# Kernel tuning notes

Measured on AMD Instinct MI355X. Metric: run time of the kernel, lower is better.

## Reference

```python
import jax, jax.numpy as jnp
import numpy as np

_EPS = 1e-5

def _ln(x, scale, shift):
    # Faithful to the module's custom layer norm: variance term is the SUM of
    # squared deviations over the feature dim (not the mean), and the affine is
    # scale * normed + shift with scale=b*, shift=s* (argument order as in source).
    m = jnp.mean(x, axis=-1, keepdims=True)
    d = x - m
    ssq = jnp.sum(d * d, axis=-1, keepdims=True)
    return scale * (d / jnp.sqrt(ssq + _EPS)) + shift


def setup_inputs() -> dict:
    key = jax.random.key(0)
    ks = jax.random.split(key, 12)
    B, T, I, H = 64, 512, 512, 512
    f32 = jnp.float32
    return {
        "x": jax.random.normal(ks[0], (B, T, I), f32),
        "hx": jax.random.normal(ks[1], (B, H), f32),
        "cx": jax.random.normal(ks[2], (B, H), f32),
        "Wi": jax.random.normal(ks[3], (4 * H, I), f32) / np.float32(np.sqrt(I)),
        "Wh": jax.random.normal(ks[4], (4 * H, H), f32) / np.float32(np.sqrt(H)),
        "bias": jax.random.normal(ks[5], (4 * H,), f32) * 0.1,
        "b1": jax.random.normal(ks[6], (4 * H,), f32) * 0.1,
        "b2": jax.random.normal(ks[7], (4 * H,), f32) * 0.1,
        "b3": jax.random.normal(ks[8], (H,), f32) * 0.1,
        "s1": 1.0 + jax.random.normal(ks[9], (4 * H,), f32) * 0.1,
        "s2": 1.0 + jax.random.normal(ks[10], (4 * H,), f32) * 0.1,
        "s3": 1.0 + jax.random.normal(ks[11], (H,), f32) * 0.1,
    }


def reference(x, hx, cx, Wi, Wh, bias, b1, b2, b3, s1, s2, s3):
    # x: [B, T, I] (batch_first). Work in time-major for the scan.
    xT = jnp.swapaxes(x, 0, 1)  # [T, B, I]
    # The input-projection layer norm has no cross-time dependency -> precompute.
    gi = _ln(jnp.einsum('tbi,gi->tbg', xT, Wi), b1, s1)  # [T, B, 4H]

    def step(carry, gi_t):
        h, c = carry
        gates = gi_t + _ln(h @ Wh.T, b2, s2) + bias  # [B, 4H]
        i, f, g, o = jnp.split(gates, 4, axis=-1)
        i = jax.nn.sigmoid(i)
        f = jax.nn.sigmoid(f)
        g = jnp.tanh(g)
        o = jax.nn.sigmoid(o)
        c_new = _ln(f * c + i * g, b3, s3)
        h_new = o * jnp.tanh(c_new)
        return (h_new, c_new), h_new

    (hy, cy), ys = jax.lax.scan(step, (hx, cx), gi)
    output = jnp.swapaxes(ys, 0, 1)  # back to [B, T, H]
    return output, hy, cy
```

## Files before the change

kernel.cpp:

```cpp
#include <hip/hip_runtime.h>
#include <cstdint>
#include <cstddef>


typedef float  f32x4 __attribute__((ext_vector_type(4)));
typedef __bf16 bf16x8 __attribute__((ext_vector_type(8)));
typedef unsigned int u32x4 __attribute__((ext_vector_type(4)));
typedef unsigned short u16x4 __attribute__((ext_vector_type(4)));

#define DEV __device__ __forceinline__

DEV unsigned short f2b(float f){
  unsigned int u = __builtin_bit_cast(unsigned int, f);
  unsigned int r = (u + 0x7FFFu + ((u >> 16) & 1u)) >> 16;
  return (unsigned short)r;
}
DEV float b2f(unsigned short s){
  unsigned int u = ((unsigned int)s) << 16;
  return __builtin_bit_cast(float, u);
}
DEV float tanh_fast(float x){
  const float e = __expf(2.f * x);
  return 1.f - 2.f * __builtin_amdgcn_rcpf(e + 1.f);
}
DEV float sigmoid_fast(float x){
  return __builtin_amdgcn_rcpf(1.f + __expf(-x));
}

__global__ __launch_bounds__(256) void conv_bf16(const float* __restrict__ src,
                                                 unsigned short* __restrict__ dst,
                                                 int n4){
  int i = blockIdx.x * 256 + threadIdx.x;
  if (i >= n4) return;
  f32x4 v = ((const f32x4*)src)[i];
  u16x4 o;
  #pragma unroll
  for (int j = 0; j < 4; ++j) o[j] = f2b(v[j]);
  ((u16x4*)dst)[i] = o;
}

__global__ __launch_bounds__(256) void init_h(const float* __restrict__ hx,
                                              unsigned long long* __restrict__ hbuf){
  int s = blockIdx.x;
  int p = threadIdx.x;
  float h0 = hx[s * 512 + 2 * p];
  float h1 = hx[s * 512 + 2 * p + 1];
  unsigned long long v = (unsigned long long)f2b(h0) |
                         ((unsigned long long)f2b(h1) << 16);
  hbuf[(size_t)s * 512 + p] = v;
}

__global__ __launch_bounds__(256, 2) void gemm_gi(const unsigned short* __restrict__ Xb,
                                                  const unsigned short* __restrict__ Wib,
                                                  unsigned short* __restrict__ Gp){
  __shared__ unsigned short As[128 * 48];
  __shared__ unsigned short Bs[128 * 48];
  const int tid = threadIdx.x;
  const int m0 = blockIdx.x * 128;
  const int n0 = blockIdx.y * 128;
  const int w = tid >> 6, lane = tid & 63;
  const int lr = lane & 15, lq = lane >> 4;
  const int wm = (w & 1) * 64, wn = (w >> 1) * 64;
  const int sr = tid >> 2;
  const int sc = (tid & 3) * 8;
  const unsigned short* gx = Xb + (size_t)(m0 + sr) * 512 + sc;
  const unsigned short* gw = Wib + (size_t)(n0 + sr) * 512 + sc;
  f32x4 acc[4][4] = {};
  for (int kb = 0; kb < 16; ++kb){
    u32x4 a0 = *(const u32x4*)(gx + kb * 32);
    u32x4 a1 = *(const u32x4*)(gx + 64 * 512 + kb * 32);
    u32x4 b0 = *(const u32x4*)(gw + kb * 32);
    u32x4 b1 = *(const u32x4*)(gw + 64 * 512 + kb * 32);
    __syncthreads();
    *(u32x4*)&As[sr * 48 + sc] = a0;
    *(u32x4*)&As[(sr + 64) * 48 + sc] = a1;
    *(u32x4*)&Bs[sr * 48 + sc] = b0;
    *(u32x4*)&Bs[(sr + 64) * 48 + sc] = b1;
    __syncthreads();
    bf16x8 af[4], bfv[4];
    #pragma unroll
    for (int mi = 0; mi < 4; ++mi) af[mi] = *(const bf16x8*)&As[(wm + mi * 16 + lr) * 48 + lq * 8];
    #pragma unroll
    for (int ni = 0; ni < 4; ++ni) bfv[ni] = *(const bf16x8*)&Bs[(wn + ni * 16 + lr) * 48 + lq * 8];
    #pragma unroll
    for (int mi = 0; mi < 4; ++mi)
      #pragma unroll
      for (int ni = 0; ni < 4; ++ni)
        acc[mi][ni] = __builtin_amdgcn_mfma_f32_16x16x32_bf16(af[mi], bfv[ni], acc[mi][ni], 0, 0, 0);
  }
  #pragma unroll
  for (int mi = 0; mi < 4; ++mi){
    const int rowb = m0 + wm + mi * 16 + lq * 4;
    #pragma unroll
    for (int ni = 0; ni < 4; ++ni){
      const int col = n0 + wn + ni * 16 + lr;
      #pragma unroll
      for (int r = 0; r < 4; ++r)
        Gp[(size_t)(rowb + r) * 2048 + col] = f2b(acc[mi][ni][r]);
    }
  }
}

__global__ __launch_bounds__(256) void ln_rows(unsigned short* __restrict__ G,
                                               const float* __restrict__ b1,
                                               const float* __restrict__ s1){
  const int row = blockIdx.x;
  const int tid = threadIdx.x;
  unsigned short* rp = G + (size_t)row * 2048 + tid * 8;
  u32x4 raw = *(const u32x4*)rp;
  float x[8];
  #pragma unroll
  for (int j = 0; j < 8; ++j){
    unsigned int word = raw[j >> 1];
    unsigned short us = (j & 1) ? (unsigned short)(word >> 16) : (unsigned short)(word & 0xFFFF);
    x[j] = b2f(us);
  }
  float s = 0.f, q = 0.f;
  #pragma unroll
  for (int j = 0; j < 8; ++j){ s += x[j]; q += x[j] * x[j]; }
  #pragma unroll
  for (int o = 1; o < 64; o <<= 1){ s += __shfl_xor(s, o); q += __shfl_xor(q, o); }
  __shared__ float ps[4][2];
  const int wv = tid >> 6;
  if ((tid & 63) == 0){ ps[wv][0] = s; ps[wv][1] = q; }
  __syncthreads();
  s = ps[0][0] + ps[1][0] + ps[2][0] + ps[3][0];
  q = ps[0][1] + ps[1][1] + ps[2][1] + ps[3][1];
  const float mu = s * (1.f / 2048.f);
  const float inv = rsqrtf((q - s * mu) + 1e-5f);
  const float* b1p = b1 + tid * 8;
  const float* s1p = s1 + tid * 8;
  u32x4 outw;
  #pragma unroll
  for (int j = 0; j < 4; ++j){
    float y0 = b1p[2 * j]     * ((x[2 * j]     - mu) * inv) + s1p[2 * j];
    float y1 = b1p[2 * j + 1] * ((x[2 * j + 1] - mu) * inv) + s1p[2 * j + 1];
    outw[j] = (unsigned int)f2b(y0) | ((unsigned int)f2b(y1) << 16);
  }
  *(u32x4*)rp = outw;
}

__global__ __launch_bounds__(512, 2) void lstm_rec(
    const unsigned short* __restrict__ Gi,
    const unsigned short* __restrict__ Whb,
    const float* __restrict__ bias,
    const float* __restrict__ b2, const float* __restrict__ s2,
    const float* __restrict__ b3, const float* __restrict__ s3,
    const float* __restrict__ cx,
    unsigned long long* __restrict__ hbuf,
    unsigned long long* __restrict__ pA,
    unsigned long long* __restrict__ pCs,
    float* __restrict__ out){
  const int tid = threadIdx.x;
  const int tm = (blockIdx.x >> 1) & 3;
  const int ks = ((blockIdx.x >> 3) << 1) | (blockIdx.x & 1);
  const int w = tid >> 6;
  const int lane = tid & 63;
  const int lr = lane & 15, lq = lane >> 4;

  const int type = w >> 1;
  const int jloc = (w & 1) * 16 + lr;
  const int row_g = type * 512 + ks * 32 + jloc;
  const float b2r = b2[row_g];
  const float sbr = s2[row_g] + bias[row_g];

  bf16x8 bfr[16];
  {
    const unsigned short* wr = Whb + (size_t)row_g * 512 + lq * 8;
    #pragma unroll
    for (int kk = 0; kk < 16; ++kk) bfr[kk] = *(const bf16x8*)(wr + kk * 32);
  }

  const int cs = tid >> 5;
  const int cj = tid & 31;
  const int hcol = ks * 32 + cj;
  const int bidx = tm * 16 + cs;
  float c_val = cx[(size_t)bidx * 512 + hcol];
  const float b3j = b3[hcol], s3j = s3[hcol];

  const int psmp = 2 * w + (lane >> 5);
  const int pidx = lane & 31;
  const int pl_slice = (lane >> 1) & 15;
  const int pl_kind  = lane & 1;

  float b3c[16], s3c[16];
  #pragma unroll
  for (int jj = 0; jj < 8; ++jj){
    const int c0 = 2 * pidx + 64 * jj;
    b3c[2 * jj]     = b3[c0];     b3c[2 * jj + 1] = b3[c0 + 1];
    s3c[2 * jj]     = s3[c0];     s3c[2 * jj + 1] = s3[c0 + 1];
  }

  __shared__ unsigned short hlds[16 * 520];
  __shared__ float act[4][32][17];
  __shared__ float redA[8][16][2];
  __shared__ float stAl[16][2];

  float cc_own = 0.f, o_own = 0.f;

  for (int t = 0; t < 512; ++t){
    float giv[4];
    #pragma unroll
    for (int r = 0; r < 4; ++r){
      const int b = tm * 16 + lq * 4 + r;
      giv[r] = b2f(Gi[((size_t)b * 512 + t) * 2048 + row_g]);
    }

    if (t == 0){
      const unsigned long long* hsrc = hbuf + (size_t)(tm * 16 + psmp) * 512;
      unsigned long long hv[8];
      for (;;){
        bool ok = true;
        #pragma unroll
        for (int j = 0; j < 8; ++j)
          hv[j] = __hip_atomic_load(hsrc + pidx + 32 * j, __ATOMIC_RELAXED, __HIP_MEMORY_SCOPE_AGENT);
        #pragma unroll
        for (int j = 0; j < 8; ++j) ok &= ((unsigned)(hv[j] >> 32) == 0u);
        if (__all((int)ok)) break;
      }
      #pragma unroll
      for (int j = 0; j < 8; ++j)
        *(unsigned int*)&hlds[psmp * 520 + 2 * (pidx + 32 * j)] = (unsigned)hv[j];
    } else {
      const unsigned int tg = (unsigned)t;
      const unsigned long long* hsrc =
          hbuf + (size_t)(t & 1) * 32768 + (size_t)(tm * 16 + psmp) * 512;
      const unsigned long long* sp =
          pCs + ((size_t)(t & 1) * 4 + tm) * 512 + pl_slice * 32 + psmp * 2 + pl_kind;
      unsigned long long hv[16];
      unsigned long long sv;
      for (;;){
        bool ok = true;
        #pragma unroll
        for (int j = 0; j < 16; ++j)
          hv[j] = __hip_atomic_load(hsrc + 2 * pidx + 64 * (j >> 1) + (j & 1),
                                    __ATOMIC_RELAXED, __HIP_MEMORY_SCOPE_AGENT);
        sv = __hip_atomic_load(sp, __ATOMIC_RELAXED, __HIP_MEMORY_SCOPE_AGENT);
        #pragma unroll
        for (int j = 0; j < 16; ++j) ok &= ((unsigned)(hv[j] >> 32) == tg);
        ok &= ((unsigned)(sv >> 32) == tg);
        if (__all((int)ok)) break;
      }
      float pv = __builtin_bit_cast(float, (unsigned)sv);
      #pragma unroll
      for (int o = 2; o < 32; o <<= 1) pv += __shfl_xor(pv, o);
      const float ov = __shfl_xor(pv, 1);
      const float S = pl_kind ? ov : pv;
      const float Q = pl_kind ? pv : ov;
      const float mu = S * (1.f / 512.f);
      const float inv = rsqrtf((Q - S * mu) + 1e-5f);
      c_val = b3j * ((cc_own - mu) * inv) + s3j;
      const float h_self = o_own * tanh_fast(c_val);
      out[((size_t)bidx * 512 + (t - 1)) * 512 + hcol] = h_self;
      #pragma unroll
      for (int jj = 0; jj < 8; ++jj){
        const unsigned long long v0 = hv[2 * jj], v1 = hv[2 * jj + 1];
        const float cc0 = b2f((unsigned short)(v0 & 0xFFFF));
        const float oo0 = b2f((unsigned short)((v0 >> 16) & 0xFFFF));
        const float cc1 = b2f((unsigned short)(v1 & 0xFFFF));
        const float oo1 = b2f((unsigned short)((v1 >> 16) & 0xFFFF));
        const float h0 = oo0 * tanh_fast(b3c[2 * jj]     * ((cc0 - mu) * inv) + s3c[2 * jj]);
        const float h1 = oo1 * tanh_fast(b3c[2 * jj + 1] * ((cc1 - mu) * inv) + s3c[2 * jj + 1]);
        *(unsigned int*)&hlds[psmp * 520 + 2 * pidx + 64 * jj] =
            (unsigned)f2b(h0) | ((unsigned)f2b(h1) << 16);
      }
    }
    __syncthreads();

    f32x4 acc = {0.f, 0.f, 0.f, 0.f};
    #pragma unroll
    for (int kk = 0; kk < 16; ++kk){
      bf16x8 af = *(const bf16x8*)&hlds[lr * 520 + lq * 8 + kk * 32];
      acc = __builtin_amdgcn_mfma_f32_16x16x32_bf16(af, bfr[kk], acc, 0, 0, 0);
    }
    #pragma unroll
    for (int r = 0; r < 4; ++r){
      float s = acc[r], q = acc[r] * acc[r];
      #pragma unroll
      for (int o = 1; o < 16; o <<= 1){ s += __shfl_xor(s, o); q += __shfl_xor(q, o); }
      if (lr == 0){ redA[w][lq * 4 + r][0] = s; redA[w][lq * 4 + r][1] = q; }
    }
    __syncthreads();

    unsigned long long* slotA = pA + ((size_t)(t & 1) * 4 + tm) * 512;
    const unsigned int atag = (unsigned)(t + 1);
    if (w == 0 && lane < 32){
      const int smp = lane >> 1, kd = lane & 1;
      float Sp = 0.f;
      #pragma unroll
      for (int w2 = 0; w2 < 8; ++w2) Sp += redA[w2][smp][kd];
      const unsigned long long pvs = ((unsigned long long)atag << 32) |
          (unsigned long long)__builtin_bit_cast(unsigned int, Sp);
      __hip_atomic_store(slotA + (size_t)ks * 32 + lane, pvs,
                         __ATOMIC_RELAXED, __HIP_MEMORY_SCOPE_AGENT);
    }
    {
      const unsigned long long* ap = slotA + pl_slice * 32 + psmp * 2 + pl_kind;
      unsigned long long av;
      for (;;){
        av = __hip_atomic_load(ap, __ATOMIC_RELAXED, __HIP_MEMORY_SCOPE_AGENT);
        if (__all((int)((unsigned)(av >> 32) == atag))) break;
      }
      float pv = __builtin_bit_cast(float, (unsigned)av);
      #pragma unroll
      for (int o = 2; o < 32; o <<= 1) pv += __shfl_xor(pv, o);
      const float ov = __shfl_xor(pv, 1);
      const float S = pl_kind ? ov : pv;
      const float Q = pl_kind ? pv : ov;
      if ((lane & 31) == 0){
        const float mu = S * (1.f / 2048.f);
        stAl[psmp][0] = mu;
        stAl[psmp][1] = rsqrtf((Q - S * mu) + 1e-5f);
      }
    }
    __syncthreads();

    #pragma unroll
    for (int r = 0; r < 4; ++r){
      const int s0 = lq * 4 + r;
      const float nv = (acc[r] - stAl[s0][0]) * stAl[s0][1];
      const float gv = giv[r] + b2r * nv + sbr;
      float a;
      if (type == 2) a = tanh_fast(gv);
      else           a = sigmoid_fast(gv);
      act[type][jloc][s0] = a;
    }
    __syncthreads();

    const float i_g = act[0][cj][cs];
    const float f_g = act[1][cj][cs];
    const float g_g = act[2][cj][cs];
    const float o_g = act[3][cj][cs];
    const float cc = f_g * c_val + i_g * g_g;
    float sC = cc, qC = cc * cc;
    #pragma unroll
    for (int o = 1; o < 32; o <<= 1){ sC += __shfl_xor(sC, o); qC += __shfl_xor(qC, o); }

    const unsigned int ntag = (unsigned)(t + 1);
    const size_t np = (size_t)((t + 1) & 1);
    unsigned long long* slotC = pCs + (np * 4 + tm) * 512;
    if ((lane & 31) < 2){
      const float v = (lane & 1) ? qC : sC;
      const unsigned long long pvs = ((unsigned long long)ntag << 32) |
          (unsigned long long)__builtin_bit_cast(unsigned int, v);
      __hip_atomic_store(slotC + (size_t)ks * 32 + cs * 2 + (lane & 1), pvs,
                         __ATOMIC_RELAXED, __HIP_MEMORY_SCOPE_AGENT);
    }
    {
      const unsigned long long pvh = ((unsigned long long)ntag << 32) |
          (unsigned long long)f2b(cc) | ((unsigned long long)f2b(o_g) << 16);
      __hip_atomic_store(hbuf + np * 32768 + (size_t)bidx * 512 + hcol, pvh,
                         __ATOMIC_RELAXED, __HIP_MEMORY_SCOPE_AGENT);
    }
    cc_own = cc; o_own = o_g;
  }

  {
    const unsigned long long* sp =
        pCs + ((size_t)0 * 4 + tm) * 512 + pl_slice * 32 + psmp * 2 + pl_kind;
    unsigned long long sv;
    for (;;){
      sv = __hip_atomic_load(sp, __ATOMIC_RELAXED, __HIP_MEMORY_SCOPE_AGENT);
      if (__all((int)((unsigned)(sv >> 32) == 512u))) break;
    }
    float pv = __builtin_bit_cast(float, (unsigned)sv);
    #pragma unroll
    for (int o = 2; o < 32; o <<= 1) pv += __shfl_xor(pv, o);
    const float ov = __shfl_xor(pv, 1);
    const float S = pl_kind ? ov : pv;
    const float Q = pl_kind ? pv : ov;
    const float mu = S * (1.f / 512.f);
    const float inv = rsqrtf((Q - S * mu) + 1e-5f);
    const float cn = b3j * ((cc_own - mu) * inv) + s3j;
    const float h = o_own * tanh_fast(cn);
    out[((size_t)bidx * 512 + 511) * 512 + hcol] = h;
    out[16777216u + (size_t)bidx * 512 + hcol] = h;
    out[16777216u + 32768u + (size_t)bidx * 512 + hcol] = cn;
  }
}

extern "C" void kernel_launch(void* const* d_in, const int* in_sizes, int n_in,
                              void* d_out, int out_size, void* d_ws, size_t ws_size,
                              hipStream_t stream){
  (void)in_sizes; (void)n_in; (void)out_size; (void)ws_size;
  const float* x    = (const float*)d_in[0];
  const float* hx   = (const float*)d_in[1];
  const float* cx   = (const float*)d_in[2];
  const float* Wi   = (const float*)d_in[3];
  const float* Wh   = (const float*)d_in[4];
  const float* bias = (const float*)d_in[5];
  const float* b1   = (const float*)d_in[6];
  const float* b2   = (const float*)d_in[7];
  const float* b3   = (const float*)d_in[8];
  const float* s1   = (const float*)d_in[9];
  const float* s2   = (const float*)d_in[10];
  const float* s3   = (const float*)d_in[11];
  float* out = (float*)d_out;
  char* ws = (char*)d_ws;

  unsigned short*     xb   = (unsigned short*)(ws);
  unsigned short*     wib  = (unsigned short*)(ws + 33554432);
  unsigned short*     whb  = (unsigned short*)(ws + 35651584);
  unsigned short*     gp   = (unsigned short*)(ws + 37748736);
  unsigned long long* hbuf = (unsigned long long*)(ws + 171966464);
  unsigned long long* pA   = (unsigned long long*)(ws + 172490752);
  unsigned long long* pCs  = (unsigned long long*)(ws + 172523520);

  hipMemsetAsync(hbuf, 0, 589824, stream);
  conv_bf16<<<16384, 256, 0, stream>>>(x,  xb,  4194304);
  conv_bf16<<<1024,  256, 0, stream>>>(Wi, wib, 262144);
  conv_bf16<<<1024,  256, 0, stream>>>(Wh, whb, 262144);
  init_h<<<64, 256, 0, stream>>>(hx, hbuf);
  gemm_gi<<<dim3(256, 16, 1), 256, 0, stream>>>(xb, wib, gp);
  ln_rows<<<32768, 256, 0, stream>>>(gp, b1, s1);
  lstm_rec<<<64, 512, 0, stream>>>(gp, whb, bias, b2, s2, b3, s3, cx,
                                   hbuf, pA, pCs, out);
}
```

Baseline: 3.590 ms.

## Group recurrent blocks per XCD and poll peers via sc0 loads

```diff
diff --git a/kernel.cpp b/kernel.cpp
--- a/kernel.cpp
+++ b/kernel.cpp
@@ -10,6 +10,14 @@
 
 #define DEV __device__ __forceinline__
 
+#define LD2_SC0(dst, p) asm volatile("global_load_dwordx2 %0, %1, off sc0" : "=v"(dst) : "v"(p))
+#define ST2_SC0(p, v)   asm volatile("global_store_dwordx2 %0, %1, off sc0" :: "v"(p), "v"(v) : "memory")
+#define LD2_MALL(dst, p) (dst) = __hip_atomic_load((p), __ATOMIC_RELAXED, __HIP_MEMORY_SCOPE_AGENT)
+#define VM0_FENCE() do{ asm volatile("s_waitcnt vmcnt(0)" ::: "memory"); \
+                        __builtin_amdgcn_sched_barrier(0); }while(0)
+
+#define NBLK 320
+
 DEV unsigned short f2b(float f){
   unsigned int u = __builtin_bit_cast(unsigned int, f);
   unsigned int r = (u + 0x7FFFu + ((u >> 16) & 1u)) >> 16;
@@ -25,6 +33,10 @@
 }
 DEV float sigmoid_fast(float x){
   return __builtin_amdgcn_rcpf(1.f + __expf(-x));
+}
+DEV void post_u64(unsigned long long* p, unsigned long long v){
+  ST2_SC0(p, v);
+  __hip_atomic_store(p, v, __ATOMIC_RELAXED, __HIP_MEMORY_SCOPE_AGENT);
 }
 
 __global__ __launch_bounds__(256) void conv_bf16(const float* __restrict__ src,
@@ -150,10 +162,47 @@
     unsigned long long* __restrict__ hbuf,
     unsigned long long* __restrict__ pA,
     unsigned long long* __restrict__ pCs,
+    unsigned int* __restrict__ form,
     float* __restrict__ out){
   const int tid = threadIdx.x;
-  const int tm = (blockIdx.x >> 1) & 3;
-  const int ks = ((blockIdx.x >> 3) << 1) | (blockIdx.x & 1);
+
+  __shared__ int s_tm, s_ks;
+  if (tid == 0){
+    const unsigned xcd = __builtin_amdgcn_s_getreg((31 << 11) | 20) & 15u;
+    const unsigned k = __hip_atomic_fetch_add(&form[xcd], 1u,
+                          __ATOMIC_RELAXED, __HIP_MEMORY_SCOPE_AGENT);
+    const unsigned c = k >> 4, m = k & 15u;
+    unsigned int* gcnt = &form[16 + xcd * 20 + c];
+    unsigned int* tqp  = &form[336 + xcd * 20 + c];
+    __hip_atomic_fetch_add(gcnt, 1u, __ATOMIC_RELAXED, __HIP_MEMORY_SCOPE_AGENT);
+    __hip_atomic_fetch_add(&form[656], 1u, __ATOMIC_RELEASE, __HIP_MEMORY_SCOPE_AGENT);
+    if (m == 0){
+      unsigned g;
+      for (;;){
+        g = __hip_atomic_load(gcnt, __ATOMIC_RELAXED, __HIP_MEMORY_SCOPE_AGENT);
+        if (g >= 16u) break;
+        unsigned a = __hip_atomic_load(&form[656], __ATOMIC_ACQUIRE, __HIP_MEMORY_SCOPE_AGENT);
+        if (a >= (unsigned)NBLK){
+          g = __hip_atomic_load(gcnt, __ATOMIC_RELAXED, __HIP_MEMORY_SCOPE_AGENT);
+          break;
+        }
+      }
+      unsigned tq = 255u;
+      if (g >= 16u)
+        tq = __hip_atomic_fetch_add(&form[657], 1u, __ATOMIC_RELAXED, __HIP_MEMORY_SCOPE_AGENT);
+      __hip_atomic_store(tqp, tq | 0x100u, __ATOMIC_RELAXED, __HIP_MEMORY_SCOPE_AGENT);
+    }
+    unsigned v;
+    do { v = __hip_atomic_load(tqp, __ATOMIC_RELAXED, __HIP_MEMORY_SCOPE_AGENT); }
+    while (!(v & 0x100u));
+    s_tm = (int)(v & 0xFFu);
+    s_ks = (int)m;
+  }
+  __syncthreads();
+  const int tm = s_tm;
+  const int ks = s_ks;
+  if (tm >= 4) return;
+
   const int w = tid >> 6;
   const int lane = tid & 63;
   const int lr = lane & 15, lq = lane >> 4;
@@ -197,6 +246,7 @@
   __shared__ float stAl[16][2];
 
   float cc_own = 0.f, o_own = 0.f;
+  bool use_mall = false;
 
   for (int t = 0; t < 512; ++t){
     float giv[4];
@@ -208,19 +258,26 @@
 
     if (t == 0){
       const unsigned long long* hsrc = hbuf + (size_t)(tm * 16 + psmp) * 512;
-      unsigned long long hv[8];
+      unsigned long long hv0[8];
+      unsigned spin = 0;
       for (;;){
+        if (!use_mall){
+          #pragma unroll
+          for (int j = 0; j < 8; ++j) LD2_SC0(hv0[j], hsrc + pidx + 32 * j);
+          VM0_FENCE();
+        } else {
+          #pragma unroll
+          for (int j = 0; j < 8; ++j) LD2_MALL(hv0[j], hsrc + pidx + 32 * j);
+        }
         bool ok = true;
         #pragma unroll
-        for (int j = 0; j < 8; ++j)
-          hv[j] = __hip_atomic_load(hsrc + pidx + 32 * j, __ATOMIC_RELAXED, __HIP_MEMORY_SCOPE_AGENT);
-        #pragma unroll
-        for (int j = 0; j < 8; ++j) ok &= ((unsigned)(hv[j] >> 32) == 0u);
+        for (int j = 0; j < 8; ++j) ok &= ((unsigned)(hv0[j] >> 32) == 0u);
         if (__all((int)ok)) break;
+        if (++spin > 64u) use_mall = true;
       }
       #pragma unroll
       for (int j = 0; j < 8; ++j)
-        *(unsigned int*)&hlds[psmp * 520 + 2 * (pidx + 32 * j)] = (unsigned)hv[j];
+        *(unsigned int*)&hlds[psmp * 520 + 2 * (pidx + 32 * j)] = (unsigned)hv0[j];
     } else {
       const unsigned int tg = (unsigned)t;
       const unsigned long long* hsrc =
@@ -229,17 +286,26 @@
           pCs + ((size_t)(t & 1) * 4 + tm) * 512 + pl_slice * 32 + psmp * 2 + pl_kind;
       unsigned long long hv[16];
       unsigned long long sv;
+      unsigned spin = 0;
       for (;;){
+        if (!use_mall){
+          #pragma unroll
+          for (int j = 0; j < 16; ++j)
+            LD2_SC0(hv[j], hsrc + 2 * pidx + 64 * (j >> 1) + (j & 1));
+          LD2_SC0(sv, sp);
+          VM0_FENCE();
+        } else {
+          #pragma unroll
+          for (int j = 0; j < 16; ++j)
+            LD2_MALL(hv[j], hsrc + 2 * pidx + 64 * (j >> 1) + (j & 1));
+          LD2_MALL(sv, sp);
+        }
         bool ok = true;
-        #pragma unroll
-        for (int j = 0; j < 16; ++j)
-          hv[j] = __hip_atomic_load(hsrc + 2 * pidx + 64 * (j >> 1) + (j & 1),
-                                    __ATOMIC_RELAXED, __HIP_MEMORY_SCOPE_AGENT);
-        sv = __hip_atomic_load(sp, __ATOMIC_RELAXED, __HIP_MEMORY_SCOPE_AGENT);
         #pragma unroll
         for (int j = 0; j < 16; ++j) ok &= ((unsigned)(hv[j] >> 32) == tg);
         ok &= ((unsigned)(sv >> 32) == tg);
         if (__all((int)ok)) break;
+        if (++spin > 64u) use_mall = true;
       }
       float pv = __builtin_bit_cast(float, (unsigned)sv);
       #pragma unroll
@@ -291,15 +357,17 @@
       for (int w2 = 0; w2 < 8; ++w2) Sp += redA[w2][smp][kd];
       const unsigned long long pvs = ((unsigned long long)atag << 32) |
           (unsigned long long)__builtin_bit_cast(unsigned int, Sp);
-      __hip_atomic_store(slotA + (size_t)ks * 32 + lane, pvs,
-                         __ATOMIC_RELAXED, __HIP_MEMORY_SCOPE_AGENT);
+      post_u64(slotA + (size_t)ks * 32 + lane, pvs);
     }
     {
       const unsigned long long* ap = slotA + pl_slice * 32 + psmp * 2 + pl_kind;
       unsigned long long av;
+      unsigned spin = 0;
       for (;;){
-        av = __hip_atomic_load(ap, __ATOMIC_RELAXED, __HIP_MEMORY_SCOPE_AGENT);
+        if (!use_mall){ LD2_SC0(av, ap); VM0_FENCE(); }
+        else          { LD2_MALL(av, ap); }
         if (__all((int)((unsigned)(av >> 32) == atag))) break;
+        if (++spin > 64u) use_mall = true;
       }
       float pv = __builtin_bit_cast(float, (unsigned)av);
       #pragma unroll
@@ -343,14 +411,12 @@
       const float v = (lane & 1) ? qC : sC;
       const unsigned long long pvs = ((unsigned long long)ntag << 32) |
           (unsigned long long)__builtin_bit_cast(unsigned int, v);
-      __hip_atomic_store(slotC + (size_t)ks * 32 + cs * 2 + (lane & 1), pvs,
-                         __ATOMIC_RELAXED, __HIP_MEMORY_SCOPE_AGENT);
+      post_u64(slotC + (size_t)ks * 32 + cs * 2 + (lane & 1), pvs);
     }
     {
       const unsigned long long pvh = ((unsigned long long)ntag << 32) |
           (unsigned long long)f2b(cc) | ((unsigned long long)f2b(o_g) << 16);
-      __hip_atomic_store(hbuf + np * 32768 + (size_t)bidx * 512 + hcol, pvh,
-                         __ATOMIC_RELAXED, __HIP_MEMORY_SCOPE_AGENT);
+      post_u64(hbuf + np * 32768 + (size_t)bidx * 512 + hcol, pvh);
     }
     cc_own = cc; o_own = o_g;
   }
@@ -359,9 +425,12 @@
     const unsigned long long* sp =
         pCs + ((size_t)0 * 4 + tm) * 512 + pl_slice * 32 + psmp * 2 + pl_kind;
     unsigned long long sv;
+    unsigned spin = 0;
     for (;;){
-      sv = __hip_atomic_load(sp, __ATOMIC_RELAXED, __HIP_MEMORY_SCOPE_AGENT);
+      if (!use_mall){ LD2_SC0(sv, sp); VM0_FENCE(); }
+      else          { LD2_MALL(sv, sp); }
       if (__all((int)((unsigned)(sv >> 32) == 512u))) break;
+      if (++spin > 64u) use_mall = true;
     }
     float pv = __builtin_bit_cast(float, (unsigned)sv);
     #pragma unroll
@@ -405,14 +474,15 @@
   unsigned long long* hbuf = (unsigned long long*)(ws + 171966464);
   unsigned long long* pA   = (unsigned long long*)(ws + 172490752);
   unsigned long long* pCs  = (unsigned long long*)(ws + 172523520);
-
-  hipMemsetAsync(hbuf, 0, 589824, stream);
+  unsigned int*       form = (unsigned int*)(ws + 172556288);
+
+  hipMemsetAsync(hbuf, 0, 593920, stream);
   conv_bf16<<<16384, 256, 0, stream>>>(x,  xb,  4194304);
   conv_bf16<<<1024,  256, 0, stream>>>(Wi, wib, 262144);
   conv_bf16<<<1024,  256, 0, stream>>>(Wh, whb, 262144);
   init_h<<<64, 256, 0, stream>>>(hx, hbuf);
   gemm_gi<<<dim3(256, 16, 1), 256, 0, stream>>>(xb, wib, gp);
   ln_rows<<<32768, 256, 0, stream>>>(gp, b1, s1);
-  lstm_rec<<<64, 512, 0, stream>>>(gp, whb, bias, b2, s2, b3, s3, cx,
-                                   hbuf, pA, pCs, out);
-}
+  lstm_rec<<<NBLK, 512, 0, stream>>>(gp, whb, bias, b2, s2, b3, s3, cx,
+                                     hbuf, pA, pCs, form, out);
+}
```

New measurement: 4.130 ms. +15.0%, slower.

## Vectorize spin-wait polling, add sleep backoff, publish h earlier, pad LDS for occupancy

Applied to the files above, without the earlier changes.

```diff
diff --git a/kernel.cpp b/kernel.cpp
--- a/kernel.cpp
+++ b/kernel.cpp
@@ -7,8 +7,13 @@
 typedef __bf16 bf16x8 __attribute__((ext_vector_type(8)));
 typedef unsigned int u32x4 __attribute__((ext_vector_type(4)));
 typedef unsigned short u16x4 __attribute__((ext_vector_type(4)));
+typedef unsigned long long u64x2 __attribute__((ext_vector_type(2)));
 
 #define DEV __device__ __forceinline__
+
+#define LD4_AGENT(dst, p) asm volatile("global_load_dwordx4 %0, %1, off sc1" : "=v"(dst) : "v"(p))
+#define VM0_FENCE() do{ asm volatile("s_waitcnt vmcnt(0)" ::: "memory"); \
+                        __builtin_amdgcn_sched_barrier(0); }while(0)
 
 DEV unsigned short f2b(float f){
   unsigned int u = __builtin_bit_cast(unsigned int, f);
@@ -195,8 +200,11 @@
   __shared__ float act[4][32][17];
   __shared__ float redA[8][16][2];
   __shared__ float stAl[16][2];
+  __shared__ char occ_pad[60 * 1024];
+  if (blockIdx.x == 0xFFFFu) occ_pad[tid] = (char)tid;
 
   float cc_own = 0.f, o_own = 0.f;
+  bool use_mall = false;
 
   for (int t = 0; t < 512; ++t){
     float giv[4];
@@ -208,19 +216,20 @@
 
     if (t == 0){
       const unsigned long long* hsrc = hbuf + (size_t)(tm * 16 + psmp) * 512;
-      unsigned long long hv[8];
+      unsigned long long hv0[8];
       for (;;){
         bool ok = true;
         #pragma unroll
         for (int j = 0; j < 8; ++j)
-          hv[j] = __hip_atomic_load(hsrc + pidx + 32 * j, __ATOMIC_RELAXED, __HIP_MEMORY_SCOPE_AGENT);
+          hv0[j] = __hip_atomic_load(hsrc + pidx + 32 * j, __ATOMIC_RELAXED, __HIP_MEMORY_SCOPE_AGENT);
         #pragma unroll
-        for (int j = 0; j < 8; ++j) ok &= ((unsigned)(hv[j] >> 32) == 0u);
+        for (int j = 0; j < 8; ++j) ok &= ((unsigned)(hv0[j] >> 32) == 0u);
         if (__all((int)ok)) break;
+        __builtin_amdgcn_s_sleep(2);
       }
       #pragma unroll
       for (int j = 0; j < 8; ++j)
-        *(unsigned int*)&hlds[psmp * 520 + 2 * (pidx + 32 * j)] = (unsigned)hv[j];
+        *(unsigned int*)&hlds[psmp * 520 + 2 * (pidx + 32 * j)] = (unsigned)hv0[j];
     } else {
       const unsigned int tg = (unsigned)t;
       const unsigned long long* hsrc =
@@ -229,17 +238,30 @@
           pCs + ((size_t)(t & 1) * 4 + tm) * 512 + pl_slice * 32 + psmp * 2 + pl_kind;
       unsigned long long hv[16];
       unsigned long long sv;
+      unsigned spin = 0;
       for (;;){
         bool ok = true;
-        #pragma unroll
-        for (int j = 0; j < 16; ++j)
-          hv[j] = __hip_atomic_load(hsrc + 2 * pidx + 64 * (j >> 1) + (j & 1),
-                                    __ATOMIC_RELAXED, __HIP_MEMORY_SCOPE_AGENT);
-        sv = __hip_atomic_load(sp, __ATOMIC_RELAXED, __HIP_MEMORY_SCOPE_AGENT);
+        if (!use_mall){
+          u64x2 t4[8];
+          #pragma unroll
+          for (int q = 0; q < 8; ++q) LD4_AGENT(t4[q], hsrc + 2 * pidx + 64 * q);
+          sv = __hip_atomic_load(sp, __ATOMIC_RELAXED, __HIP_MEMORY_SCOPE_AGENT);
+          VM0_FENCE();
+          #pragma unroll
+          for (int q = 0; q < 8; ++q){ hv[2 * q] = t4[q].x; hv[2 * q + 1] = t4[q].y; }
+        } else {
+          #pragma unroll
+          for (int j = 0; j < 16; ++j)
+            hv[j] = __hip_atomic_load(hsrc + 2 * pidx + 64 * (j >> 1) + (j & 1),
+                                      __ATOMIC_RELAXED, __HIP_MEMORY_SCOPE_AGENT);
+          sv = __hip_atomic_load(sp, __ATOMIC_RELAXED, __HIP_MEMORY_SCOPE_AGENT);
+        }
         #pragma unroll
         for (int j = 0; j < 16; ++j) ok &= ((unsigned)(hv[j] >> 32) == tg);
         ok &= ((unsigned)(sv >> 32) == tg);
         if (__all((int)ok)) break;
+        if (++spin > 48u) use_mall = true;
+        __builtin_amdgcn_s_sleep(2);
       }
       float pv = __builtin_bit_cast(float, (unsigned)sv);
       #pragma unroll
@@ -300,6 +322,7 @@
       for (;;){
         av = __hip_atomic_load(ap, __ATOMIC_RELAXED, __HIP_MEMORY_SCOPE_AGENT);
         if (__all((int)((unsigned)(av >> 32) == atag))) break;
+        __builtin_amdgcn_s_sleep(2);
       }
       float pv = __builtin_bit_cast(float, (unsigned)av);
       #pragma unroll
@@ -332,12 +355,17 @@
     const float g_g = act[2][cj][cs];
     const float o_g = act[3][cj][cs];
     const float cc = f_g * c_val + i_g * g_g;
-    float sC = cc, qC = cc * cc;
-    #pragma unroll
-    for (int o = 1; o < 32; o <<= 1){ sC += __shfl_xor(sC, o); qC += __shfl_xor(qC, o); }
-
     const unsigned int ntag = (unsigned)(t + 1);
     const size_t np = (size_t)((t + 1) & 1);
+    {
+      const unsigned long long pvh = ((unsigned long long)ntag << 32) |
+          (unsigned long long)f2b(cc) | ((unsigned long long)f2b(o_g) << 16);
+      __hip_atomic_store(hbuf + np * 32768 + (size_t)bidx * 512 + hcol, pvh,
+                         __ATOMIC_RELAXED, __HIP_MEMORY_SCOPE_AGENT);
+    }
+    float sC = cc, qC = cc * cc;
+    #pragma unroll
+    for (int o = 1; o < 32; o <<= 1){ sC += __shfl_xor(sC, o); qC += __shfl_xor(qC, o); }
     unsigned long long* slotC = pCs + (np * 4 + tm) * 512;
     if ((lane & 31) < 2){
       const float v = (lane & 1) ? qC : sC;
@@ -346,12 +374,6 @@
       __hip_atomic_store(slotC + (size_t)ks * 32 + cs * 2 + (lane & 1), pvs,
                          __ATOMIC_RELAXED, __HIP_MEMORY_SCOPE_AGENT);
     }
-    {
-      const unsigned long long pvh = ((unsigned long long)ntag << 32) |
-          (unsigned long long)f2b(cc) | ((unsigned long long)f2b(o_g) << 16);
-      __hip_atomic_store(hbuf + np * 32768 + (size_t)bidx * 512 + hcol, pvh,
-                         __ATOMIC_RELAXED, __HIP_MEMORY_SCOPE_AGENT);
-    }
     cc_own = cc; o_own = o_g;
   }
 
@@ -362,6 +384,7 @@
     for (;;){
       sv = __hip_atomic_load(sp, __ATOMIC_RELAXED, __HIP_MEMORY_SCOPE_AGENT);
       if (__all((int)((unsigned)(sv >> 32) == 512u))) break;
+      __builtin_amdgcn_s_sleep(2);
     }
     float pv = __builtin_bit_cast(float, (unsigned)sv);
     #pragma unroll
```

Result: faster. 2.969 ms (-17.3%).

## Replace per-element tagged h exchange with per-block flags plus bulk payload loads

Applied to the files above, without the earlier changes.

```diff
diff --git a/kernel.cpp b/kernel.cpp
--- a/kernel.cpp
+++ b/kernel.cpp
@@ -9,6 +9,10 @@
 typedef unsigned short u16x4 __attribute__((ext_vector_type(4)));
 
 #define DEV __device__ __forceinline__
+
+#define LD4_AGENT(dst, p) asm volatile("global_load_dwordx4 %0, %1, off sc1" : "=v"(dst) : "v"(p))
+#define VM0_FENCE() do{ asm volatile("s_waitcnt vmcnt(0)" ::: "memory"); \
+                        __builtin_amdgcn_sched_barrier(0); }while(0)
 
 DEV unsigned short f2b(float f){
   unsigned int u = __builtin_bit_cast(unsigned int, f);
@@ -37,17 +41,6 @@
   #pragma unroll
   for (int j = 0; j < 4; ++j) o[j] = f2b(v[j]);
   ((u16x4*)dst)[i] = o;
-}
-
-__global__ __launch_bounds__(256) void init_h(const float* __restrict__ hx,
-                                              unsigned long long* __restrict__ hbuf){
-  int s = blockIdx.x;
-  int p = threadIdx.x;
-  float h0 = hx[s * 512 + 2 * p];
-  float h1 = hx[s * 512 + 2 * p + 1];
-  unsigned long long v = (unsigned long long)f2b(h0) |
-                         ((unsigned long long)f2b(h1) << 16);
-  hbuf[(size_t)s * 512 + p] = v;
 }
 
 __global__ __launch_bounds__(256, 2) void gemm_gi(const unsigned short* __restrict__ Xb,
@@ -146,8 +139,10 @@
     const float* __restrict__ bias,
     const float* __restrict__ b2, const float* __restrict__ s2,
     const float* __restrict__ b3, const float* __restrict__ s3,
+    const float* __restrict__ hx,
     const float* __restrict__ cx,
-    unsigned long long* __restrict__ hbuf,
+    unsigned int* __restrict__ hbuf,
+    unsigned long long* __restrict__ pF,
     unsigned long long* __restrict__ pA,
     unsigned long long* __restrict__ pCs,
     float* __restrict__ out){
@@ -185,11 +180,13 @@
 
   float b3c[16], s3c[16];
   #pragma unroll
-  for (int jj = 0; jj < 8; ++jj){
-    const int c0 = 2 * pidx + 64 * jj;
-    b3c[2 * jj]     = b3[c0];     b3c[2 * jj + 1] = b3[c0 + 1];
-    s3c[2 * jj]     = s3[c0];     s3c[2 * jj + 1] = s3[c0 + 1];
-  }
+  for (int q = 0; q < 4; ++q)
+    #pragma unroll
+    for (int j = 0; j < 4; ++j){
+      const int c = 4 * pidx + 128 * q + j;
+      b3c[4 * q + j] = b3[c];
+      s3c[4 * q + j] = s3[c];
+    }
 
   __shared__ unsigned short hlds[16 * 520];
   __shared__ float act[4][32][17];
@@ -207,40 +204,34 @@
     }
 
     if (t == 0){
-      const unsigned long long* hsrc = hbuf + (size_t)(tm * 16 + psmp) * 512;
-      unsigned long long hv[8];
-      for (;;){
-        bool ok = true;
+      const float* hr = hx + (size_t)(tm * 16 + psmp) * 512;
+      #pragma unroll
+      for (int q = 0; q < 4; ++q){
+        f32x4 hv4 = *(const f32x4*)(hr + 4 * pidx + 128 * q);
+        unsigned long long pk = 0;
         #pragma unroll
-        for (int j = 0; j < 8; ++j)
-          hv[j] = __hip_atomic_load(hsrc + pidx + 32 * j, __ATOMIC_RELAXED, __HIP_MEMORY_SCOPE_AGENT);
-        #pragma unroll
-        for (int j = 0; j < 8; ++j) ok &= ((unsigned)(hv[j] >> 32) == 0u);
-        if (__all((int)ok)) break;
+        for (int j = 0; j < 4; ++j)
+          pk |= (unsigned long long)f2b(hv4[j]) << (16 * j);
+        *(unsigned long long*)&hlds[psmp * 520 + 4 * pidx + 128 * q] = pk;
       }
-      #pragma unroll
-      for (int j = 0; j < 8; ++j)
-        *(unsigned int*)&hlds[psmp * 520 + 2 * (pidx + 32 * j)] = (unsigned)hv[j];
     } else {
       const unsigned int tg = (unsigned)t;
-      const unsigned long long* hsrc =
-          hbuf + (size_t)(t & 1) * 32768 + (size_t)(tm * 16 + psmp) * 512;
+      const unsigned long long* fp = pF + (size_t)(t & 1) * 64 + tm * 16 + (lane & 15);
       const unsigned long long* sp =
           pCs + ((size_t)(t & 1) * 4 + tm) * 512 + pl_slice * 32 + psmp * 2 + pl_kind;
-      unsigned long long hv[16];
       unsigned long long sv;
       for (;;){
-        bool ok = true;
-        #pragma unroll
-        for (int j = 0; j < 16; ++j)
-          hv[j] = __hip_atomic_load(hsrc + 2 * pidx + 64 * (j >> 1) + (j & 1),
-                                    __ATOMIC_RELAXED, __HIP_MEMORY_SCOPE_AGENT);
+        unsigned long long fv = __hip_atomic_load(fp, __ATOMIC_RELAXED, __HIP_MEMORY_SCOPE_AGENT);
         sv = __hip_atomic_load(sp, __ATOMIC_RELAXED, __HIP_MEMORY_SCOPE_AGENT);
-        #pragma unroll
-        for (int j = 0; j < 16; ++j) ok &= ((unsigned)(hv[j] >> 32) == tg);
-        ok &= ((unsigned)(sv >> 32) == tg);
+        bool ok = ((unsigned)fv == tg) & ((unsigned)(sv >> 32) == tg);
         if (__all((int)ok)) break;
+        __builtin_amdgcn_s_sleep(1);
       }
+      const unsigned int* hsrc =
+          hbuf + (size_t)(t & 1) * 32768 + (size_t)(tm * 16 + psmp) * 512;
+      u32x4 pay[4];
+      #pragma unroll
+      for (int q = 0; q < 4; ++q) LD4_AGENT(pay[q], hsrc + 4 * pidx + 128 * q);
       float pv = __builtin_bit_cast(float, (unsigned)sv);
       #pragma unroll
       for (int o = 2; o < 32; o <<= 1) pv += __shfl_xor(pv, o);
@@ -252,17 +243,19 @@
       c_val = b3j * ((cc_own - mu) * inv) + s3j;
       const float h_self = o_own * tanh_fast(c_val);
       out[((size_t)bidx * 512 + (t - 1)) * 512 + hcol] = h_self;
-      #pragma unroll
-      for (int jj = 0; jj < 8; ++jj){
-        const unsigned long long v0 = hv[2 * jj], v1 = hv[2 * jj + 1];
-        const float cc0 = b2f((unsigned short)(v0 & 0xFFFF));
-        const float oo0 = b2f((unsigned short)((v0 >> 16) & 0xFFFF));
-        const float cc1 = b2f((unsigned short)(v1 & 0xFFFF));
-        const float oo1 = b2f((unsigned short)((v1 >> 16) & 0xFFFF));
-        const float h0 = oo0 * tanh_fast(b3c[2 * jj]     * ((cc0 - mu) * inv) + s3c[2 * jj]);
-        const float h1 = oo1 * tanh_fast(b3c[2 * jj + 1] * ((cc1 - mu) * inv) + s3c[2 * jj + 1]);
-        *(unsigned int*)&hlds[psmp * 520 + 2 * pidx + 64 * jj] =
-            (unsigned)f2b(h0) | ((unsigned)f2b(h1) << 16);
+      VM0_FENCE();
+      #pragma unroll
+      for (int q = 0; q < 4; ++q){
+        unsigned long long pk = 0;
+        #pragma unroll
+        for (int j = 0; j < 4; ++j){
+          const unsigned int v = pay[q][j];
+          const float ccv = b2f((unsigned short)(v & 0xFFFF));
+          const float oov = b2f((unsigned short)(v >> 16));
+          const float h = oov * tanh_fast(b3c[4 * q + j] * ((ccv - mu) * inv) + s3c[4 * q + j]);
+          pk |= (unsigned long long)f2b(h) << (16 * j);
+        }
+        *(unsigned long long*)&hlds[psmp * 520 + 4 * pidx + 128 * q] = pk;
       }
     }
     __syncthreads();
@@ -300,6 +293,7 @@
       for (;;){
         av = __hip_atomic_load(ap, __ATOMIC_RELAXED, __HIP_MEMORY_SCOPE_AGENT);
         if (__all((int)((unsigned)(av >> 32) == atag))) break;
+        __builtin_amdgcn_s_sleep(2);
       }
       float pv = __builtin_bit_cast(float, (unsigned)av);
       #pragma unroll
@@ -332,12 +326,16 @@
     const float g_g = act[2][cj][cs];
     const float o_g = act[3][cj][cs];
     const float cc = f_g * c_val + i_g * g_g;
-    float sC = cc, qC = cc * cc;
-    #pragma unroll
-    for (int o = 1; o < 32; o <<= 1){ sC += __shfl_xor(sC, o); qC += __shfl_xor(qC, o); }
-
     const unsigned int ntag = (unsigned)(t + 1);
     const size_t np = (size_t)((t + 1) & 1);
+    {
+      const unsigned int pv32 = (unsigned int)f2b(cc) | ((unsigned int)f2b(o_g) << 16);
+      __hip_atomic_store(hbuf + np * 32768 + (size_t)bidx * 512 + hcol, pv32,
+                         __ATOMIC_RELAXED, __HIP_MEMORY_SCOPE_AGENT);
+    }
+    float sC = cc, qC = cc * cc;
+    #pragma unroll
+    for (int o = 1; o < 32; o <<= 1){ sC += __shfl_xor(sC, o); qC += __shfl_xor(qC, o); }
     unsigned long long* slotC = pCs + (np * 4 + tm) * 512;
     if ((lane & 31) < 2){
       const float v = (lane & 1) ? qC : sC;
@@ -346,12 +344,11 @@
       __hip_atomic_store(slotC + (size_t)ks * 32 + cs * 2 + (lane & 1), pvs,
                          __ATOMIC_RELAXED, __HIP_MEMORY_SCOPE_AGENT);
     }
-    {
-      const unsigned long long pvh = ((unsigned long long)ntag << 32) |
-          (unsigned long long)f2b(cc) | ((unsigned long long)f2b(o_g) << 16);
-      __hip_atomic_store(hbuf + np * 32768 + (size_t)bidx * 512 + hcol, pvh,
+    VM0_FENCE();
+    __syncthreads();
+    if (tid == 0)
+      __hip_atomic_store(pF + np * 64 + tm * 16 + ks, (unsigned long long)ntag,
                          __ATOMIC_RELAXED, __HIP_MEMORY_SCOPE_AGENT);
-    }
     cc_own = cc; o_own = o_g;
   }
 
@@ -362,6 +359,7 @@
     for (;;){
       sv = __hip_atomic_load(sp, __ATOMIC_RELAXED, __HIP_MEMORY_SCOPE_AGENT);
       if (__all((int)((unsigned)(sv >> 32) == 512u))) break;
+      __builtin_amdgcn_s_sleep(2);
     }
     float pv = __builtin_bit_cast(float, (unsigned)sv);
     #pragma unroll
@@ -402,17 +400,17 @@
   unsigned short*     wib  = (unsigned short*)(ws + 33554432);
   unsigned short*     whb  = (unsigned short*)(ws + 35651584);
   unsigned short*     gp   = (unsigned short*)(ws + 37748736);
-  unsigned long long* hbuf = (unsigned long long*)(ws + 171966464);
+  unsigned int*       hbuf = (unsigned int*)(ws + 171966464);
+  unsigned long long* pF   = (unsigned long long*)(ws + 172228608);
   unsigned long long* pA   = (unsigned long long*)(ws + 172490752);
   unsigned long long* pCs  = (unsigned long long*)(ws + 172523520);
 
-  hipMemsetAsync(hbuf, 0, 589824, stream);
+  hipMemsetAsync(pF, 0, 327680, stream);
   conv_bf16<<<16384, 256, 0, stream>>>(x,  xb,  4194304);
   conv_bf16<<<1024,  256, 0, stream>>>(Wi, wib, 262144);
   conv_bf16<<<1024,  256, 0, stream>>>(Wh, whb, 262144);
-  init_h<<<64, 256, 0, stream>>>(hx, hbuf);
   gemm_gi<<<dim3(256, 16, 1), 256, 0, stream>>>(xb, wib, gp);
   ln_rows<<<32768, 256, 0, stream>>>(gp, b1, s1);
-  lstm_rec<<<64, 512, 0, stream>>>(gp, whb, bias, b2, s2, b3, s3, cx,
-                                   hbuf, pA, pCs, out);
-}
+  lstm_rec<<<64, 512, 0, stream>>>(gp, whb, bias, b2, s2, b3, s3, hx, cx,
+                                   hbuf, pF, pA, pCs, out);
+}
```

After: 3.245 ms, median of 2. -9.6%, faster.
